# Performance work log

Hardware: AMD Instinct MI355X
Metric: run time of the kernel (lower is better)

Reference implementation:

```python
import jax, jax.numpy as jnp
import numpy as np

B, T, HID, H, Dk, Dv, K = 2, 1024, 1024, 8, 128, 128, 4
EPS = 1e-5


def _dwconv_causal(y, w, b):
    # y: [B,T,C], w: [C,1,K], b: [C]; torch Conv1d(padding=K-1) then [:, :, :T] == causal left-pad
    C = y.shape[-1]
    z = jnp.transpose(y, (0, 2, 1))  # [B,C,T]
    z = jax.lax.conv_general_dilated(
        z, w, window_strides=(1,), padding=[(K - 1, 0)],
        feature_group_count=C, dimension_numbers=("NCH", "OIH", "NCH"))
    z = z + b[None, :, None]
    return jnp.transpose(z, (0, 2, 1))


def _forward(x, Wq, Wk, Wv, conv_q_w, conv_q_b, conv_k_w, conv_k_b,
             conv_v_w, conv_v_b, Wa, ba, Wb, bb, Wg, Wo, ln_g, ln_b):
    b_, t_ = x.shape[0], x.shape[1]
    q = jax.nn.silu(_dwconv_causal(x @ Wq, conv_q_w, conv_q_b))
    k = jax.nn.silu(_dwconv_causal(x @ Wk, conv_k_w, conv_k_b))
    v = jax.nn.silu(_dwconv_causal(x @ Wv, conv_v_w, conv_v_b))
    q = q.reshape(b_, t_, H, Dk)
    k = k.reshape(b_, t_, H, Dk) * (Dk ** -0.5)
    v = v.reshape(b_, t_, H, Dv)
    alpha = jax.nn.sigmoid(x @ Wa + ba)  # [B,T,H]
    beta = jax.nn.sigmoid(x @ Wb + bb)   # [B,T,H]

    # time-major for scan
    qt = jnp.transpose(q, (1, 0, 2, 3))  # [T,B,H,Dk]
    kt = jnp.transpose(k, (1, 0, 2, 3))
    vt = jnp.transpose(v, (1, 0, 2, 3))  # [T,B,H,Dv]
    at = jnp.transpose(alpha, (1, 0, 2))  # [T,B,H]
    bt = jnp.transpose(beta, (1, 0, 2))

    def step(S, inp):
        q_t, k_t, v_t, a_t, b_t = inp
        sk = jnp.einsum('bhij,bhj->bhi', S, k_t)          # S @ k
        err = sk - v_t                                     # [B,H,Dv]
        S = a_t[:, :, None, None] * S - b_t[:, :, None, None] * (err[..., None] * k_t[:, :, None, :])
        o_t = jnp.einsum('bhij,bhj->bhi', S, q_t)          # S @ q (post-update)
        return S, o_t

    S0 = jnp.zeros((b_, H, Dv, Dk), x.dtype)
    _, o = jax.lax.scan(step, S0, (qt, kt, vt, at, bt))
    o = jnp.transpose(o, (1, 0, 2, 3))  # [B,T,H,Dv]

    # LayerNorm over Dv
    mu = jnp.mean(o, axis=-1, keepdims=True)
    var = jnp.mean((o - mu) ** 2, axis=-1, keepdims=True)
    o = (o - mu) * jax.lax.rsqrt(var + EPS) * ln_g + ln_b

    g = jax.nn.sigmoid(x @ Wg).reshape(b_, t_, H, Dv)
    o = (o * g).reshape(b_, t_, H * Dv)
    return o @ Wo


def setup_inputs() -> dict:
    key = jax.random.key(0)
    ks = jax.random.split(key, 18)
    s = 0.02

    def n(k, shape, scale=s):
        return jax.random.normal(k, shape, jnp.float32) * scale

    return {
        "x": jax.random.normal(ks[0], (B, T, HID), jnp.float32),
        "Wq": n(ks[1], (HID, H * Dk)),
        "Wk": n(ks[2], (HID, H * Dk)),
        "Wv": n(ks[3], (HID, H * Dv)),
        "conv_q_w": n(ks[4], (H * Dk, 1, K), 0.25),
        "conv_q_b": n(ks[5], (H * Dk,), 0.1),
        "conv_k_w": n(ks[6], (H * Dk, 1, K), 0.25),
        "conv_k_b": n(ks[7], (H * Dk,), 0.1),
        "conv_v_w": n(ks[8], (H * Dv, 1, K), 0.25),
        "conv_v_b": n(ks[9], (H * Dv,), 0.1),
        "Wa": n(ks[10], (HID, H)),
        "ba": n(ks[11], (H,), 0.1),
        "Wb": n(ks[12], (HID, H)),
        "bb": n(ks[13], (H,), 0.1),
        "Wg": n(ks[14], (HID, H * Dv)),
        "Wo": n(ks[15], (H * Dv, HID)),
        "ln_g": jnp.ones((Dv,), jnp.float32),
        "ln_b": jnp.zeros((Dv,), jnp.float32),
    }


def reference(x, Wq, Wk, Wv, conv_q_w, conv_q_b, conv_k_w, conv_k_b,
              conv_v_w, conv_v_b, Wa, ba, Wb, bb, Wg, Wo, ln_g, ln_b):
    return _forward(x, Wq, Wk, Wv, conv_q_w, conv_q_b, conv_k_w, conv_k_b,
                    conv_v_w, conv_v_b, Wa, ba, Wb, bb, Wg, Wo, ln_g, ln_b)
```

## Files before the change

### kernel.cpp

```cpp
#include <hip/hip_runtime.h>

#define TSEQ 1024
#define HID_ 1024
#define NH 8
#define DK 128
#define DV 128
#define ROWS 2048
#define SZf (ROWS * HID_)
#define LCH 64
#define NCK 16
#define KSTR 136
#define ESTR 65

typedef __attribute__((ext_vector_type(8))) short short8;
typedef __attribute__((ext_vector_type(4))) float f32x4;
#define MFMA __builtin_amdgcn_mfma_f32_16x16x32_bf16

__device__ __forceinline__ float sig_(float x) { return 1.f / (1.f + __expf(-x)); }

__device__ __forceinline__ ushort f2bf(float f) {
    unsigned int u = __builtin_bit_cast(unsigned int, f);
    u += 0x7FFF + ((u >> 16) & 1);
    return (ushort)(u >> 16);
}
__device__ __forceinline__ float bf2f(ushort u) {
    return __builtin_bit_cast(float, ((unsigned int)u) << 16);
}
__device__ __forceinline__ unsigned int pk2(float lo, float hi) {
    return (unsigned int)f2bf(lo) | ((unsigned int)f2bf(hi) << 16);
}

__global__ __launch_bounds__(256)
void k_x2bf(const float* __restrict__ x, ushort* __restrict__ xb)
{
    const size_t i8 = (size_t)blockIdx.x * 256 + threadIdx.x;
    float4 v0 = *(const float4*)(x + i8 * 8);
    float4 v1 = *(const float4*)(x + i8 * 8 + 4);
    uint4 o;
    o.x = pk2(v0.x, v0.y); o.y = pk2(v0.z, v0.w);
    o.z = pk2(v1.x, v1.y); o.w = pk2(v1.z, v1.w);
    *(uint4*)(xb + i8 * 8) = o;
}

__global__ __launch_bounds__(256)
void k_wT(const float* __restrict__ s0, const float* __restrict__ s1,
          const float* __restrict__ s2, const float* __restrict__ s3,
          ushort* __restrict__ dst)
{
    const int z = blockIdx.z;
    const float* W = (z == 0) ? s0 : (z == 1) ? s1 : (z == 2) ? s2 : s3;
    ushort* WT = dst + (size_t)z * (1024 * 1024);
    __shared__ float t[64][65];
    const int n0 = blockIdx.x * 64, k0 = blockIdx.y * 64;
    const int rr = threadIdx.x >> 4, cc = threadIdx.x & 15;
#pragma unroll
    for (int i = 0; i < 4; ++i) {
        const int row = i * 16 + rr;
        float4 v = *(const float4*)(W + (size_t)(k0 + row) * 1024 + n0 + cc * 4);
        t[row][cc * 4 + 0] = v.x; t[row][cc * 4 + 1] = v.y;
        t[row][cc * 4 + 2] = v.z; t[row][cc * 4 + 3] = v.w;
    }
    __syncthreads();
#pragma unroll
    for (int i = 0; i < 4; ++i) {
        const int n = i * 16 + rr;
        const int kc = cc * 4;
        ushort4 o;
        o.x = f2bf(t[kc + 0][n]); o.y = f2bf(t[kc + 1][n]);
        o.z = f2bf(t[kc + 2][n]); o.w = f2bf(t[kc + 3][n]);
        *(ushort4*)(WT + (size_t)(n0 + n) * 1024 + k0 + kc) = o;
    }
}

#define LDSB 40
__device__ __forceinline__ void gemm_tile_mfma(const ushort* __restrict__ A,
                                               const ushort* __restrict__ BT,
                                               float* __restrict__ C,
                                               int brow, int bcol)
{
    __shared__ ushort As[128 * LDSB];
    __shared__ ushort Bs[128 * LDSB];
    const int tid  = threadIdx.x;
    const int lane = tid & 63;
    const int wv   = tid >> 6;
    const int wm   = (wv >> 1) * 64;
    const int wn   = (wv & 1) * 64;
    const int l15  = lane & 15;
    const int k8   = (lane >> 4) * 8;
    const int srow = tid >> 1;
    const int skh  = (tid & 1) * 16;

    f32x4 acc[4][4];
#pragma unroll
    for (int i = 0; i < 4; ++i)
#pragma unroll
        for (int j = 0; j < 4; ++j)
#pragma unroll
            for (int e = 0; e < 4; ++e) acc[i][j][e] = 0.f;

    const ushort* arow = A  + (size_t)(brow + srow) * 1024 + skh;
    const ushort* brp  = BT + (size_t)(bcol + srow) * 1024 + skh;
    ushort* asw = As + srow * LDSB + skh;
    ushort* bsw = Bs + srow * LDSB + skh;

    for (int k0 = 0; k0 < 1024; k0 += 32) {
        uint4 a0 = *(const uint4*)(arow + k0);
        uint4 a1 = *(const uint4*)(arow + k0 + 8);
        uint4 b0 = *(const uint4*)(brp + k0);
        uint4 b1 = *(const uint4*)(brp + k0 + 8);
        __syncthreads();
        *(uint4*)(asw)     = a0;
        *(uint4*)(asw + 8) = a1;
        *(uint4*)(bsw)     = b0;
        *(uint4*)(bsw + 8) = b1;
        __syncthreads();
        short8 af[4], bf[4];
#pragma unroll
        for (int i = 0; i < 4; ++i)
            af[i] = *(const short8*)(As + (wm + i * 16 + l15) * LDSB + k8);
#pragma unroll
        for (int j = 0; j < 4; ++j)
            bf[j] = *(const short8*)(Bs + (wn + j * 16 + l15) * LDSB + k8);
#pragma unroll
        for (int i = 0; i < 4; ++i)
#pragma unroll
            for (int j = 0; j < 4; ++j)
                acc[i][j] = MFMA(af[i], bf[j], acc[i][j], 0, 0, 0);
    }
    const int l4 = lane >> 4;
#pragma unroll
    for (int i = 0; i < 4; ++i)
#pragma unroll
        for (int j = 0; j < 4; ++j)
#pragma unroll
            for (int r = 0; r < 4; ++r)
                C[(size_t)(brow + wm + i * 16 + l4 * 4 + r) * 1024 +
                  bcol + wn + j * 16 + l15] = acc[i][j][r];
}

__global__ __launch_bounds__(256)
void k_gemm4(const ushort* __restrict__ A, const ushort* __restrict__ WT,
             float* __restrict__ Cbase)
{
    const ushort* BT = WT + (size_t)blockIdx.z * (1024 * 1024);
    float* C = Cbase + (size_t)blockIdx.z * SZf;
    gemm_tile_mfma(A, BT, C, blockIdx.y * 128, blockIdx.x * 128);
}

__global__ __launch_bounds__(256)
void k_gemm1(const ushort* __restrict__ A, const ushort* __restrict__ BT,
             float* __restrict__ C)
{
    gemm_tile_mfma(A, BT, C, blockIdx.y * 128, blockIdx.x * 128);
}

__global__ __launch_bounds__(64)
void k_ab(const float* __restrict__ x, const float* __restrict__ Wa,
          const float* __restrict__ ba, const float* __restrict__ Wb,
          const float* __restrict__ bb, float* __restrict__ aT,
          float* __restrict__ bT)
{
    const int r = blockIdx.x;
    const int lane = threadIdx.x;
    const int b = r >> 10, t = r & 1023;
    const float* xr = x + (size_t)r * HID_;
    float acc[16];
#pragma unroll
    for (int n = 0; n < 16; ++n) acc[n] = 0.f;
    for (int c = lane; c < HID_; c += 64) {
        const float xv = xr[c];
        const float* wa = Wa + c * 8;
        const float* wb = Wb + c * 8;
#pragma unroll
        for (int n = 0; n < 8; ++n) {
            acc[n]     = fmaf(xv, wa[n], acc[n]);
            acc[8 + n] = fmaf(xv, wb[n], acc[8 + n]);
        }
    }
#pragma unroll
    for (int n = 0; n < 16; ++n) {
#pragma unroll
        for (int m = 32; m; m >>= 1) acc[n] += __shfl_xor(acc[n], m);
    }
    if (lane < 8) {
        aT[(size_t)(b * 8 + lane) * TSEQ + t] = sig_(acc[lane] + ba[lane]);
        bT[(size_t)(b * 8 + lane) * TSEQ + t] = sig_(acc[8 + lane] + bb[lane]);
    }
}

__global__ __launch_bounds__(256)
void k_conv_save(const float* __restrict__ q, const float* __restrict__ k,
                 const float* __restrict__ v, float* __restrict__ scr)
{
    const int z = blockIdx.z, b = blockIdx.y, j = blockIdx.x + 1;
    const float* y = (z == 0) ? q : (z == 1) ? k : v;
    float* d = scr + ((size_t)(z * 2 + b) * 15 + (j - 1)) * 3 * 1024;
    const float* s = y + ((size_t)b * TSEQ + j * 64 - 3) * HID_;
    for (int i = threadIdx.x; i < 3 * 1024; i += 256)
        d[i] = s[i];
}

__global__ __launch_bounds__(256)
void k_conv_apply(float* __restrict__ q, float* __restrict__ k, float* __restrict__ v,
                  const float* __restrict__ scr,
                  const float* __restrict__ wq, const float* __restrict__ bq,
                  const float* __restrict__ wk, const float* __restrict__ bk,
                  const float* __restrict__ wv, const float* __restrict__ bv)
{
    const int z = blockIdx.z, b = blockIdx.y;
    const int j = blockIdx.x >> 2, cg = blockIdx.x & 3;
    float* y          = (z == 0) ? q  : (z == 1) ? k  : v;
    const float* w    = (z == 0) ? wq : (z == 1) ? wk : wv;
    const float* bias = (z == 0) ? bq : (z == 1) ? bk : bv;
    const float scale = (z == 1) ? 0.08838834764831845f : 1.f;
    const int c = cg * 256 + threadIdx.x;
    const float w0 = w[c * 4], w1 = w[c * 4 + 1], w2 = w[c * 4 + 2], w3 = w[c * 4 + 3];
    const float bs = bias[c];
    float y0 = 0.f, y1 = 0.f, y2 = 0.f;
    if (j > 0) {
        const float* s = scr + ((size_t)(z * 2 + b) * 15 + (j - 1)) * 3 * 1024 + c;
        y0 = s[0]; y1 = s[1024]; y2 = s[2048];
    }
    float* yp = y + ((size_t)b * TSEQ + j * 64) * HID_ + c;
#pragma unroll 4
    for (int t = 0; t < 64; ++t) {
        float y3  = yp[(size_t)t * HID_];
        float acc = fmaf(w0, y0, fmaf(w1, y1, fmaf(w2, y2, fmaf(w3, y3, bs))));
        float sv  = acc * sig_(acc) * scale;
        yp[(size_t)t * HID_] = sv;
        y0 = y1; y1 = y2; y2 = y3;
    }
}

__global__ __launch_bounds__(256)
void k_stageprep(const float* __restrict__ klin, const float* __restrict__ qlin,
                 const float* __restrict__ vlin,
                 const float* __restrict__ aT, const float* __restrict__ bT,
                 ushort* __restrict__ Kst, ushort* __restrict__ Qst,
                 ushort* __restrict__ Vst, ushort* __restrict__ KTst,
                 ushort* __restrict__ Mg, ushort* __restrict__ Gg,
                 float* __restrict__ pug, float* __restrict__ pog,
                 float* __restrict__ cg, float* __restrict__ dtotg)
{
    const int cid = blockIdx.x;
    const int bh = cid >> 4, c = cid & 15;
    const int b = bh >> 3, h = bh & 7;
    const int tid = threadIdx.x;
    const int t0 = c * LCH;

    __shared__ ushort Kb[64 * KSTR], Qb[64 * KSTR];
    __shared__ ushort Vl[128 * 72];
    __shared__ float Ef[64 * ESTR];
    __shared__ float Mf[64 * ESTR];
    __shared__ float cums[64], bv[64];

    if (tid < 64) {
        const float a = aT[(size_t)bh * TSEQ + t0 + tid];
        bv[tid] = bT[(size_t)bh * TSEQ + t0 + tid];
        float cs = __logf(a);
#pragma unroll
        for (int d = 1; d < 64; d <<= 1) {
            float pv = __shfl_up(cs, d);
            if (tid >= d) cs += pv;
        }
        cums[tid] = cs;
    }
    const float* kb = klin + ((size_t)b * TSEQ + t0) * HID_ + h * DK;
    const float* qb = qlin + ((size_t)b * TSEQ + t0) * HID_ + h * DK;
    const float* vb = vlin + ((size_t)b * TSEQ + t0) * HID_ + h * DV;
    const size_t go = (size_t)cid * 8192;
#pragma unroll
    for (int j = 0; j < 8; ++j) {
        const int i4 = tid + j * 256;
        const int row = i4 >> 5, c4 = i4 & 31;
        float4 kv = *(const float4*)(kb + (size_t)row * HID_ + c4 * 4);
        float4 qv = *(const float4*)(qb + (size_t)row * HID_ + c4 * 4);
        float4 vv = *(const float4*)(vb + (size_t)row * HID_ + c4 * 4);
        uint2 kp; kp.x = pk2(kv.x, kv.y); kp.y = pk2(kv.z, kv.w);
        uint2 qp; qp.x = pk2(qv.x, qv.y); qp.y = pk2(qv.z, qv.w);
        *(uint2*)(Kst + go + row * 128 + c4 * 4) = kp;
        *(uint2*)(Qst + go + row * 128 + c4 * 4) = qp;
        *(uint2*)(Kb + row * KSTR + c4 * 4) = kp;
        *(uint2*)(Qb + row * KSTR + c4 * 4) = qp;
        const int dv0 = c4 * 4;
        Vl[(dv0 + 0) * 72 + row] = f2bf(vv.x);
        Vl[(dv0 + 1) * 72 + row] = f2bf(vv.y);
        Vl[(dv0 + 2) * 72 + row] = f2bf(vv.z);
        Vl[(dv0 + 3) * 72 + row] = f2bf(vv.w);
    }
    __syncthreads();

#pragma unroll
    for (int j = 0; j < 4; ++j) {
        const int idx = tid + j * 256;
        const int dv = idx >> 3, tq = (idx & 7) * 8;
        *(uint4*)(Vst + go + dv * 64 + tq) = *(const uint4*)(Vl + dv * 72 + tq);
        const int dk = idx >> 3, tt = (idx & 7) * 8;
        ushort tmp[8];
#pragma unroll
        for (int e = 0; e < 8; ++e) tmp[e] = Kb[(tt + e) * KSTR + dk];
        *(uint4*)(KTst + go + dk * 64 + tt) = *(uint4*)tmp;
    }

    const int wv = tid >> 6, l = tid & 63, l15 = l & 15, lq = l >> 4;
    const int k8o = lq * 8;
    f32x4 accK[4], accQ4[4];
#pragma unroll
    for (int j = 0; j < 4; ++j) {
        accK[j] = f32x4{0.f, 0.f, 0.f, 0.f};
        accQ4[j] = f32x4{0.f, 0.f, 0.f, 0.f};
    }
#pragma unroll
    for (int kk = 0; kk < 4; ++kk) {
        short8 aK = *(const short8*)(Kb + (wv * 16 + l15) * KSTR + kk * 32 + k8o);
        short8 aQ = *(const short8*)(Qb + (wv * 16 + l15) * KSTR + kk * 32 + k8o);
#pragma unroll
        for (int js = 0; js < 4; ++js) {
            short8 bK = *(const short8*)(Kb + (js * 16 + l15) * KSTR + kk * 32 + k8o);
            accK[js]  = MFMA(aK, bK, accK[js], 0, 0, 0);
            accQ4[js] = MFMA(aQ, bK, accQ4[js], 0, 0, 0);
        }
    }
    ushort* Gc = Gg + (size_t)cid * 4096;
#pragma unroll
    for (int js = 0; js < 4; ++js) {
#pragma unroll
        for (int r = 0; r < 4; ++r) {
            const int t = wv * 16 + lq * 4 + r;
            const int s = js * 16 + l15;
            const float cp = (t > 0) ? cums[t - 1] : 0.f;
            Ef[t * ESTR + s] = (s < t) ? __expf(cp - cums[s]) * accK[js][r] : 0.f;
            const float gv = (s <= t) ? __expf(cums[t] - cums[s]) * accQ4[js][r] : 0.f;
            Gc[t * 64 + s] = f2bf(gv);
        }
    }
    __syncthreads();

    if (tid < 64) {
        const int s = tid;
        for (int r = 0; r < 64; ++r) Mf[r * ESTR + s] = 0.f;
        Mf[s * ESTR + s] = bv[s];
        for (int t = 1; t < 64; ++t) {
            float s0 = 0.f, s1 = 0.f;
            int r = 0;
            for (; r + 1 < t; r += 2) {
                s0 = fmaf(Ef[t * ESTR + r],     Mf[r * ESTR + s],       s0);
                s1 = fmaf(Ef[t * ESTR + r + 1], Mf[(r + 1) * ESTR + s], s1);
            }
            if (r < t) s0 = fmaf(Ef[t * ESTR + r], Mf[r * ESTR + s], s0);
            if (s < t) Mf[t * ESTR + s] = -bv[t] * (s0 + s1);
        }
    }
    __syncthreads();
    ushort* Mc = Mg + (size_t)cid * 4096;
#pragma unroll
    for (int j = 0; j < 16; ++j) {
        const int e = tid + j * 256;
        Mc[e] = f2bf(Mf[(e >> 6) * ESTR + (e & 63)]);
    }
    if (tid < 64) {
        const float cp = (tid > 0) ? cums[tid - 1] : 0.f;
        pug[cid * 64 + tid] = __expf(cp);
        pog[cid * 64 + tid] = __expf(cums[tid]);
        cg [cid * 64 + tid] = __expf(cums[63] - cums[tid]);
        if (tid == 0) dtotg[cid] = __expf(cums[63]);
    }
}

__global__ __launch_bounds__(256)
void k_scan2(const ushort* __restrict__ Kst, const ushort* __restrict__ KTst,
             const ushort* __restrict__ Vst, const ushort* __restrict__ Mg,
             const float* __restrict__ pug, const float* __restrict__ cgd,
             const float* __restrict__ dtg,
             ushort* __restrict__ Sst, ushort* __restrict__ Wst)
{
    const int blk = blockIdx.x;
    const int bh = blk >> 1, half = blk & 1;
    const int tid = threadIdx.x;
    const int wv = tid >> 6, l = tid & 63, l15 = l & 15, lq = l >> 4;
    const int k8o = lq * 8;
    const int dvw = wv * 16;

    __shared__ ushort Kb[64 * KSTR];
    __shared__ ushort KTb[128 * 72];
    __shared__ ushort Mb[64 * 72];
    __shared__ ushort Vb[64 * 72];
    __shared__ ushort Shb[64 * KSTR], Slb[64 * KSTR];
    __shared__ ushort Yb[64 * 72], Wb[64 * 72], Wcb[64 * 72];
    __shared__ float puv[64], cv2[64], dts[1];

    f32x4 accS[8];
#pragma unroll
    for (int m = 0; m < 8; ++m) accS[m] = f32x4{0.f, 0.f, 0.f, 0.f};

    uint4 rk[4], rkt[4], rm[2], rv[2];
    float rpu = 0.f, rcv = 0.f, rdt = 0.f;

    auto LOADC = [&](int cc) {
        const int cid = bh * 16 + cc;
        const size_t go = (size_t)cid * 8192;
#pragma unroll
        for (int j = 0; j < 4; ++j) {
            rk[j]  = *(const uint4*)(Kst  + go + (tid + j * 256) * 8);
            rkt[j] = *(const uint4*)(KTst + go + (tid + j * 256) * 8);
        }
#pragma unroll
        for (int j = 0; j < 2; ++j) {
            rm[j] = *(const uint4*)(Mg + (size_t)cid * 4096 + (tid + j * 256) * 8);
            rv[j] = *(const uint4*)(Vst + go + half * 4096 + (tid + j * 256) * 8);
        }
        if (tid < 64) {
            rpu = pug[cid * 64 + tid];
            rcv = cgd[cid * 64 + tid];
            if (tid == 0) rdt = dtg[cid];
        }
    };
    auto WRITEC = [&]() {
#pragma unroll
        for (int j = 0; j < 4; ++j) {
            const int i16 = tid + j * 256;
            *(uint4*)(Kb  + (i16 >> 4) * KSTR + (i16 & 15) * 8) = rk[j];
            *(uint4*)(KTb + (i16 >> 3) * 72   + (i16 & 7) * 8)  = rkt[j];
        }
#pragma unroll
        for (int j = 0; j < 2; ++j) {
            const int i8 = tid + j * 256;
            *(uint4*)(Mb + (i8 >> 3) * 72 + (i8 & 7) * 8) = rm[j];
            *(uint4*)(Vb + (i8 >> 3) * 72 + (i8 & 7) * 8) = rv[j];
        }
        if (tid < 64) {
            puv[tid] = rpu; cv2[tid] = rcv;
            if (tid == 0) dts[0] = rdt;
        }
    };

    LOADC(0); WRITEC();
    __syncthreads();

    for (int c = 0; c < NCK; ++c) {
        if (c + 1 < NCK) LOADC(c + 1);

#pragma unroll
        for (int m = 0; m < 8; ++m) {
            ushort h4[4], l4v[4];
#pragma unroll
            for (int r = 0; r < 4; ++r) {
                const float sv = accS[m][r];
                const ushort hi = f2bf(sv);
                h4[r] = hi;
                l4v[r] = f2bf(sv - bf2f(hi));
            }
            *(uint2*)(Shb + (dvw + l15) * KSTR + m * 16 + lq * 4) = *(uint2*)h4;
            *(uint2*)(Slb + (dvw + l15) * KSTR + m * 16 + lq * 4) = *(uint2*)l4v;
        }
        f32x4 accU[4];
#pragma unroll
        for (int jj = 0; jj < 4; ++jj) accU[jj] = f32x4{0.f, 0.f, 0.f, 0.f};
#pragma unroll
        for (int kk = 0; kk < 4; ++kk) {
            short8 sh = *(const short8*)(Shb + (dvw + l15) * KSTR + kk * 32 + k8o);
            short8 sl = *(const short8*)(Slb + (dvw + l15) * KSTR + kk * 32 + k8o);
#pragma unroll
            for (int jj = 0; jj < 4; ++jj) {
                short8 ka = *(const short8*)(Kb + (jj * 16 + l15) * KSTR + kk * 32 + k8o);
                accU[jj] = MFMA(ka, sh, accU[jj], 0, 0, 0);
                accU[jj] = MFMA(ka, sl, accU[jj], 0, 0, 0);
            }
        }
#pragma unroll
        for (int jj = 0; jj < 4; ++jj) {
            float pu4[4];
            *(float4*)pu4 = *(const float4*)(puv + jj * 16 + lq * 4);
            ushort v4[4];
            *(uint2*)v4 = *(const uint2*)(Vb + (dvw + l15) * 72 + jj * 16 + lq * 4);
            ushort y4[4];
#pragma unroll
            for (int r = 0; r < 4; ++r)
                y4[r] = f2bf(bf2f(v4[r]) - pu4[r] * accU[jj][r]);
            *(uint2*)(Yb + (dvw + l15) * 72 + jj * 16 + lq * 4) = *(uint2*)y4;
        }
        f32x4 accW[4];
#pragma unroll
        for (int jj = 0; jj < 4; ++jj) accW[jj] = f32x4{0.f, 0.f, 0.f, 0.f};
#pragma unroll
        for (int kk = 0; kk < 2; ++kk) {
            short8 yb = *(const short8*)(Yb + (dvw + l15) * 72 + kk * 32 + k8o);
#pragma unroll
            for (int jj = 0; jj < 4; ++jj) {
                short8 mf = *(const short8*)(Mb + (jj * 16 + l15) * 72 + kk * 32 + k8o);
                accW[jj] = MFMA(mf, yb, accW[jj], 0, 0, 0);
            }
        }
#pragma unroll
        for (int jj = 0; jj < 4; ++jj) {
            float cv4[4];
            *(float4*)cv4 = *(const float4*)(cv2 + jj * 16 + lq * 4);
            ushort w4[4], wc4[4];
#pragma unroll
            for (int r = 0; r < 4; ++r) {
                const float wl = accW[jj][r];
                w4[r]  = f2bf(wl);
                wc4[r] = f2bf(wl * cv4[r]);
            }
            *(uint2*)(Wb  + (dvw + l15) * 72 + jj * 16 + lq * 4) = *(uint2*)w4;
            *(uint2*)(Wcb + (dvw + l15) * 72 + jj * 16 + lq * 4) = *(uint2*)wc4;
        }
        const float dt = dts[0];
#pragma unroll
        for (int m = 0; m < 8; ++m)
#pragma unroll
            for (int r = 0; r < 4; ++r) accS[m][r] *= dt;
#pragma unroll
        for (int kk = 0; kk < 2; ++kk) {
            short8 wc = *(const short8*)(Wcb + (dvw + l15) * 72 + kk * 32 + k8o);
#pragma unroll
            for (int m = 0; m < 8; ++m) {
                short8 kt = *(const short8*)(KTb + (m * 16 + l15) * 72 + kk * 32 + k8o);
                accS[m] = MFMA(kt, wc, accS[m], 0, 0, 0);
            }
        }
        {
            const int cid = bh * 16 + c;
#pragma unroll
            for (int j = 0; j < 4; ++j) {
                const int idx = l + j * 64;
                const int dvo = idx >> 4, ko = (idx & 15) * 8;
                *(uint4*)(Sst + (size_t)cid * 16384 +
                          (half * 64 + dvw + dvo) * 128 + ko) =
                    *(const uint4*)(Shb + (dvw + dvo) * KSTR + ko);
            }
#pragma unroll
            for (int j = 0; j < 2; ++j) {
                const int idx = l + j * 64;
                const int dvo = idx >> 3, t8 = (idx & 7) * 8;
                *(uint4*)(Wst + (size_t)cid * 8192 +
                          (half * 64 + dvw + dvo) * 64 + t8) =
                    *(const uint4*)(Wb + (dvw + dvo) * 72 + t8);
            }
        }
        __syncthreads();
        if (c + 1 < NCK) WRITEC();
        __syncthreads();
    }
}

__global__ __launch_bounds__(256)
void k_out(const ushort* __restrict__ Sst, const ushort* __restrict__ Qst,
           const ushort* __restrict__ Gg, const ushort* __restrict__ Wst,
           const float* __restrict__ pog, const float* __restrict__ g_lin,
           const float* __restrict__ lng, const float* __restrict__ lnb,
           ushort* __restrict__ ogb)
{
    const int cid = blockIdx.x;
    const int bh = cid >> 4, c = cid & 15;
    const int b = bh >> 3, h = bh & 7;
    const int t0 = c * LCH;
    const int tid = threadIdx.x;
    const int wv = tid >> 6, l = tid & 63, l15 = l & 15, lq = l >> 4;
    const int k8o = lq * 8;

    __shared__ ushort Sb[128 * KSTR];
    __shared__ ushort Qb[64 * KSTR];
    __shared__ ushort Gb[64 * 72];
    __shared__ ushort Wqb[128 * 72];
    __shared__ float  Ot[64 * 132];
    __shared__ float  pov[64];

#pragma unroll
    for (int j = 0; j < 8; ++j) {
        const int i16 = tid + j * 256;
        *(uint4*)(Sb + (i16 >> 4) * KSTR + (i16 & 15) * 8) =
            *(const uint4*)(Sst + (size_t)cid * 16384 + i16 * 8);
    }
#pragma unroll
    for (int j = 0; j < 4; ++j) {
        const int i16 = tid + j * 256;
        *(uint4*)(Qb + (i16 >> 4) * KSTR + (i16 & 15) * 8) =
            *(const uint4*)(Qst + (size_t)cid * 8192 + i16 * 8);
        const int i8 = i16;
        *(uint4*)(Wqb + (i8 >> 3) * 72 + (i8 & 7) * 8) =
            *(const uint4*)(Wst + (size_t)cid * 8192 + i8 * 8);
    }
#pragma unroll
    for (int j = 0; j < 2; ++j) {
        const int i8 = tid + j * 256;
        *(uint4*)(Gb + (i8 >> 3) * 72 + (i8 & 7) * 8) =
            *(const uint4*)(Gg + (size_t)cid * 4096 + i8 * 8);
    }
    if (tid < 64) pov[tid] = pog[cid * 64 + tid];
    __syncthreads();

#pragma unroll
    for (int i = 0; i < 2; ++i) {
        const int dvt = wv * 2 + i;
        f32x4 acc[4], acg[4];
#pragma unroll
        for (int jj = 0; jj < 4; ++jj) {
            acc[jj] = f32x4{0.f, 0.f, 0.f, 0.f};
            acg[jj] = f32x4{0.f, 0.f, 0.f, 0.f};
        }
#pragma unroll
        for (int kk = 0; kk < 4; ++kk) {
            short8 sa = *(const short8*)(Sb + (dvt * 16 + l15) * KSTR + kk * 32 + k8o);
#pragma unroll
            for (int jj = 0; jj < 4; ++jj) {
                short8 qb = *(const short8*)(Qb + (jj * 16 + l15) * KSTR + kk * 32 + k8o);
                acc[jj] = MFMA(sa, qb, acc[jj], 0, 0, 0);
            }
        }
#pragma unroll
        for (int kk = 0; kk < 2; ++kk) {
            short8 wa = *(const short8*)(Wqb + (dvt * 16 + l15) * 72 + kk * 32 + k8o);
#pragma unroll
            for (int jj = 0; jj < 4; ++jj) {
                short8 gb = *(const short8*)(Gb + (jj * 16 + l15) * 72 + kk * 32 + k8o);
                acg[jj] = MFMA(wa, gb, acg[jj], 0, 0, 0);
            }
        }
#pragma unroll
        for (int jj = 0; jj < 4; ++jj) {
            const int t = jj * 16 + l15;
            const float po = pov[t];
            float4 o4;
            o4.x = po * acc[jj][0] + acg[jj][0];
            o4.y = po * acc[jj][1] + acg[jj][1];
            o4.z = po * acc[jj][2] + acg[jj][2];
            o4.w = po * acc[jj][3] + acg[jj][3];
            *(float4*)(Ot + t * 132 + dvt * 16 + lq * 4) = o4;
        }
    }
    __syncthreads();

    const int d = l * 2;
    const float lg0 = lng[d], lg1 = lng[d + 1];
    const float lb0 = lnb[d], lb1 = lnb[d + 1];
    const size_t btbase = (size_t)b * TSEQ + t0 + wv * 16;
#pragma unroll 1
    for (int rr = 0; rr < 16; ++rr) {
        const int t = wv * 16 + rr;
        float2 xv = *(const float2*)(Ot + t * 132 + d);
        float s = xv.x + xv.y;
#pragma unroll
        for (int m = 32; m; m >>= 1) s += __shfl_xor(s, m);
        const float mu = s * (1.f / 128.f);
        const float d0 = xv.x - mu, d1 = xv.y - mu;
        float v = d0 * d0 + d1 * d1;
#pragma unroll
        for (int m = 32; m; m >>= 1) v += __shfl_xor(v, m);
        const float inv = rsqrtf(v * (1.f / 128.f) + 1e-5f);
        const float* gp = g_lin + (btbase + rr) * HID_ + h * DV;
        const float g0 = sig_(gp[d]), g1 = sig_(gp[d + 1]);
        const float y0 = (d0 * inv * lg0 + lb0) * g0;
        const float y1 = (d1 * inv * lg1 + lb1) * g1;
        *(uint*)(ogb + (btbase + rr) * HID_ + h * DV + d) = pk2(y0, y1);
    }
}

extern "C" void kernel_launch(void* const* d_in, const int* in_sizes, int n_in,
                              void* d_out, int out_size, void* d_ws, size_t ws_size,
                              hipStream_t stream)
{
    const float* x   = (const float*)d_in[0];
    const float* Wq  = (const float*)d_in[1];
    const float* Wk  = (const float*)d_in[2];
    const float* Wv  = (const float*)d_in[3];
    const float* cqw = (const float*)d_in[4];
    const float* cqb = (const float*)d_in[5];
    const float* ckw = (const float*)d_in[6];
    const float* ckb = (const float*)d_in[7];
    const float* cvw = (const float*)d_in[8];
    const float* cvb = (const float*)d_in[9];
    const float* Wa  = (const float*)d_in[10];
    const float* ba  = (const float*)d_in[11];
    const float* Wb  = (const float*)d_in[12];
    const float* bb  = (const float*)d_in[13];
    const float* Wg  = (const float*)d_in[14];
    const float* Wo  = (const float*)d_in[15];
    const float* lng = (const float*)d_in[16];
    const float* lnb = (const float*)d_in[17];
    float* out = (float*)d_out;
    float* ws  = (float*)d_ws;

    float* q_lin = ws;
    float* k_lin = ws + 1 * (size_t)SZf;
    float* v_lin = ws + 2 * (size_t)SZf;
    float* g_lin = ws + 3 * (size_t)SZf;
    float* o_buf = ws + 4 * (size_t)SZf;
    float* aT    = ws + 5 * (size_t)SZf;
    float* bT    = aT + 16 * TSEQ;
    float* pug   = bT + 16 * TSEQ;
    float* pog   = pug + 256 * 64;
    float* cgd   = pog + 256 * 64;
    float* dtg   = cgd + 256 * 64;

    float*  tail = ws + 5 * (size_t)SZf + 131072;
    ushort* Kst  = (ushort*)tail;
    ushort* Qst  = Kst + (size_t)256 * 8192;
    ushort* xbf  = Qst + (size_t)256 * 8192;
    ushort* Vst  = xbf;
    ushort* KTst = xbf + (size_t)256 * 8192;

    ushort* WT4 = (ushort*)o_buf;
    ushort* WoT = (ushort*)k_lin;
    ushort* ogb = (ushort*)q_lin;
    ushort* Sst = (ushort*)o_buf;
    ushort* Mg  = (ushort*)out;
    ushort* Gg  = Mg + (size_t)256 * 4096;
    ushort* Wst = Gg + (size_t)256 * 4096;

    k_x2bf<<<1024, 256, 0, stream>>>(x, xbf);
    k_wT<<<dim3(16, 16, 4), 256, 0, stream>>>(Wq, Wk, Wv, Wg, WT4);
    k_gemm4<<<dim3(8, 16, 4), 256, 0, stream>>>(xbf, WT4, ws);
    k_ab<<<ROWS, 64, 0, stream>>>(x, Wa, ba, Wb, bb, aT, bT);
    k_conv_save<<<dim3(15, 2, 3), 256, 0, stream>>>(q_lin, k_lin, v_lin, o_buf);
    k_conv_apply<<<dim3(64, 2, 3), 256, 0, stream>>>(q_lin, k_lin, v_lin, o_buf,
                                                     cqw, cqb, ckw, ckb, cvw, cvb);
    k_stageprep<<<256, 256, 0, stream>>>(k_lin, q_lin, v_lin, aT, bT,
                                         Kst, Qst, Vst, KTst, Mg, Gg,
                                         pug, pog, cgd, dtg);
    k_wT<<<dim3(16, 16, 1), 256, 0, stream>>>(Wo, Wo, Wo, Wo, WoT);
    k_scan2<<<32, 256, 0, stream>>>(Kst, KTst, Vst, Mg, pug, cgd, dtg, Sst, Wst);
    k_out<<<256, 256, 0, stream>>>(Sst, Qst, Gg, Wst, pog, g_lin, lng, lnb, ogb);
    k_gemm1<<<dim3(8, 16), 256, 0, stream>>>(ogb, WoT, out);
}
```

Before: 231.4 us.

## Load GEMM tiles directly to LDS and pack four rows per k_ab block

The MFMA GEMM tile loader now uses global_load_lds, a direct global-to-LDS DMA, in place of register-staged loads and LDS stores. The LDS layout drops its padding from a stride of 40 to an unpadded 32, which may add bank conflicts on the fragment reads. Separately, k_ab now handles four rows per 256-thread block, so it launches 512 blocks instead of 2048 single-wave blocks. The aim is to cut VGPR traffic and instruction count in the GEMM load path and reduce block launch overhead in k_ab.

Measured after the change: 231.3 us. Within noise of the previous version (-0.0%).

```diff
diff --git a/kernel.cpp b/kernel.cpp
--- a/kernel.cpp
+++ b/kernel.cpp
@@ -30,6 +30,12 @@
     return (unsigned int)f2bf(lo) | ((unsigned int)f2bf(hi) << 16);
 }
 
+__device__ __forceinline__ void gload16(const void* g, void* l) {
+    __builtin_amdgcn_global_load_lds(
+        (const __attribute__((address_space(1))) unsigned int*)g,
+        (__attribute__((address_space(3))) unsigned int*)l, 16, 0, 0);
+}
+
 __global__ __launch_bounds__(256)
 void k_x2bf(const float* __restrict__ x, ushort* __restrict__ xb)
 {
@@ -72,14 +78,13 @@
     }
 }
 
-#define LDSB 40
 __device__ __forceinline__ void gemm_tile_mfma(const ushort* __restrict__ A,
                                                const ushort* __restrict__ BT,
                                                float* __restrict__ C,
                                                int brow, int bcol)
 {
-    __shared__ ushort As[128 * LDSB];
-    __shared__ ushort Bs[128 * LDSB];
+    __shared__ ushort As[128 * 32];
+    __shared__ ushort Bs[128 * 32];
     const int tid  = threadIdx.x;
     const int lane = tid & 63;
     const int wv   = tid >> 6;
@@ -87,8 +92,8 @@
     const int wn   = (wv & 1) * 64;
     const int l15  = lane & 15;
     const int k8   = (lane >> 4) * 8;
-    const int srow = tid >> 1;
-    const int skh  = (tid & 1) * 16;
+    const int row0 = (tid >> 2);
+    const int q0   = (tid & 3) * 8;
 
     f32x4 acc[4][4];
 #pragma unroll
@@ -98,29 +103,25 @@
 #pragma unroll
             for (int e = 0; e < 4; ++e) acc[i][j][e] = 0.f;
 
-    const ushort* arow = A  + (size_t)(brow + srow) * 1024 + skh;
-    const ushort* brp  = BT + (size_t)(bcol + srow) * 1024 + skh;
-    ushort* asw = As + srow * LDSB + skh;
-    ushort* bsw = Bs + srow * LDSB + skh;
-
     for (int k0 = 0; k0 < 1024; k0 += 32) {
-        uint4 a0 = *(const uint4*)(arow + k0);
-        uint4 a1 = *(const uint4*)(arow + k0 + 8);
-        uint4 b0 = *(const uint4*)(brp + k0);
-        uint4 b1 = *(const uint4*)(brp + k0 + 8);
         __syncthreads();
-        *(uint4*)(asw)     = a0;
-        *(uint4*)(asw + 8) = a1;
-        *(uint4*)(bsw)     = b0;
-        *(uint4*)(bsw + 8) = b1;
+#pragma unroll
+        for (int j = 0; j < 2; ++j) {
+            const int i   = j * 256 + tid;
+            const int row = j * 64 + row0;
+            const int i0  = j * 256 + wv * 64;
+            gload16(A  + (size_t)(brow + row) * 1024 + k0 + q0, As + i0 * 8);
+            gload16(BT + (size_t)(bcol + row) * 1024 + k0 + q0, Bs + i0 * 8);
+            (void)i;
+        }
         __syncthreads();
         short8 af[4], bf[4];
 #pragma unroll
         for (int i = 0; i < 4; ++i)
-            af[i] = *(const short8*)(As + (wm + i * 16 + l15) * LDSB + k8);
+            af[i] = *(const short8*)(As + (wm + i * 16 + l15) * 32 + k8);
 #pragma unroll
         for (int j = 0; j < 4; ++j)
-            bf[j] = *(const short8*)(Bs + (wn + j * 16 + l15) * LDSB + k8);
+            bf[j] = *(const short8*)(Bs + (wn + j * 16 + l15) * 32 + k8);
 #pragma unroll
         for (int i = 0; i < 4; ++i)
 #pragma unroll
@@ -154,14 +155,14 @@
     gemm_tile_mfma(A, BT, C, blockIdx.y * 128, blockIdx.x * 128);
 }
 
-__global__ __launch_bounds__(64)
+__global__ __launch_bounds__(256)
 void k_ab(const float* __restrict__ x, const float* __restrict__ Wa,
           const float* __restrict__ ba, const float* __restrict__ Wb,
           const float* __restrict__ bb, float* __restrict__ aT,
           float* __restrict__ bT)
 {
-    const int r = blockIdx.x;
-    const int lane = threadIdx.x;
+    const int r = blockIdx.x * 4 + (threadIdx.x >> 6);
+    const int lane = threadIdx.x & 63;
     const int b = r >> 10, t = r & 1023;
     const float* xr = x + (size_t)r * HID_;
     float acc[16];
@@ -711,7 +712,7 @@
     k_x2bf<<<1024, 256, 0, stream>>>(x, xbf);
     k_wT<<<dim3(16, 16, 4), 256, 0, stream>>>(Wq, Wk, Wv, Wg, WT4);
     k_gemm4<<<dim3(8, 16, 4), 256, 0, stream>>>(xbf, WT4, ws);
-    k_ab<<<ROWS, 64, 0, stream>>>(x, Wa, ba, Wb, bb, aT, bT);
+    k_ab<<<512, 256, 0, stream>>>(x, Wa, ba, Wb, bb, aT, bT);
     k_conv_save<<<dim3(15, 2, 3), 256, 0, stream>>>(q_lin, k_lin, v_lin, o_buf);
     k_conv_apply<<<dim3(64, 2, 3), 256, 0, stream>>>(q_lin, k_lin, v_lin, o_buf,
                                                      cqw, cqb, ckw, ckb, cvw, cvb);
```
